# Performance work log

Measured on AMD Instinct MI355X. Metric: run time of the kernel, lower is better.

The kernel has to match this reference:

```python
import jax, jax.numpy as jnp
from jax import lax
import numpy as np

B, T = 16, 256
E, H, V = 512, 1024, 32000

def setup_inputs() -> dict:
    key = jax.random.key(0)
    ks = jax.random.split(key, 10)
    s = lambda fan_in: 1.0 / np.sqrt(fan_in)
    return {
        "z": jax.random.normal(ks[0], (B, H), dtype=jnp.float32),
        "x": jax.random.randint(ks[1], (B, T), 0, V, dtype=jnp.int64),
        "emb_table": jax.random.normal(ks[2], (V, E), dtype=jnp.float32) * 0.02,
        "W_init": jax.random.uniform(ks[3], (H, H), jnp.float32, -s(H), s(H)),
        "b_init": jnp.zeros((H,), jnp.float32),
        "W_ih": jax.random.uniform(ks[4], (3 * H, E), jnp.float32, -s(H), s(H)),
        "W_hh": jax.random.uniform(ks[5], (3 * H, H), jnp.float32, -s(H), s(H)),
        "b_ih": jax.random.uniform(ks[6], (3 * H,), jnp.float32, -s(H), s(H)),
        "b_hh": jax.random.uniform(ks[7], (3 * H,), jnp.float32, -s(H), s(H)),
        "W_out": jax.random.uniform(ks[8], (V, H), jnp.float32, -s(H), s(H)),
        "b_out": jnp.zeros((V,), jnp.float32),
    }

def reference(z, x, emb_table, W_init, b_init, W_ih, W_hh, b_ih, b_hh, W_out, b_out):
    # h0 = tanh(aff_init_lm(z))
    h0 = jnp.tanh(z @ W_init.T + b_init)  # [B, H]
    xe = emb_table[x]                      # [B, T, E] embedding lookup
    # Precompute input-side gate projections for all timesteps (no recurrence on input side)
    gi_all = jnp.einsum('bte,ge->btg', xe, W_ih) + b_ih  # [B, T, 3H]

    def step(h, gi):
        gh = h @ W_hh.T + b_hh                 # [B, 3H]
        ir, iz, inn = jnp.split(gi, 3, axis=-1)
        hr, hz, hn = jnp.split(gh, 3, axis=-1)
        r = jax.nn.sigmoid(ir + hr)
        zg = jax.nn.sigmoid(iz + hz)
        n = jnp.tanh(inn + r * hn)
        h_new = (1.0 - zg) * n + zg * h
        # Original module emits aff_out_x(h[j]) (state BEFORE consuming token j),
        # so we output the PREVIOUS hidden state at each step.
        return h_new, h

    _, hs_prev = lax.scan(step, h0, jnp.swapaxes(gi_all, 0, 1))  # [T, B, H] = h0..h_{T-1}
    hs = jnp.swapaxes(hs_prev, 0, 1)                              # [B, T, H]
    logits = jnp.einsum('bth,vh->btv', hs, W_out) + b_out         # [B, T, V]
    return logits
```

## Files before the change

### kernel.cpp

```cpp
#include <hip/hip_runtime.h>

typedef __attribute__((ext_vector_type(8))) short bf16x8;
typedef __attribute__((ext_vector_type(8))) unsigned short ushort8;
typedef __attribute__((ext_vector_type(4))) float f32x4;
typedef __attribute__((ext_vector_type(4))) int i32x4;

__device__ __forceinline__ unsigned short f2bf(float f) {
  union { float f; unsigned u; } v; v.f = f;
  unsigned r = (v.u + 0x7FFFu + ((v.u >> 16) & 1u)) >> 16;
  return (unsigned short)r;
}
__device__ __forceinline__ float bf2f(unsigned short h) {
  union { unsigned u; float f; } v; v.u = ((unsigned)h) << 16;
  return v.f;
}
__device__ __forceinline__ float sigm(float x) { return 1.f / (1.f + __expf(-x)); }
__device__ __forceinline__ float tanh_(float x) { return 1.f - 2.f / (__expf(2.f * x) + 1.f); }

__device__ __forceinline__ i32x4 ld_coh_b128(const void* p) {
  i32x4 r;
  asm volatile("global_load_dwordx4 %0, %1, off sc0 sc1" : "=v"(r) : "v"(p) : "memory");
  return r;
}
__device__ __forceinline__ void st_coh_b128(void* p, i32x4 v) {
  asm volatile("global_store_dwordx4 %0, %1, off sc0 sc1" :: "v"(p), "v"(v) : "memory");
}
__device__ __forceinline__ void st_coh_b16(void* p, unsigned v) {
  asm volatile("global_store_short %0, %1, off sc0 sc1" :: "v"(p), "v"(v) : "memory");
}
__device__ __forceinline__ void wait_vm0_fence() {
  asm volatile("s_waitcnt vmcnt(0)" ::: "memory");
  __builtin_amdgcn_sched_barrier(0);
}

#define GLDS(g, l) __builtin_amdgcn_global_load_lds( \
    (const __attribute__((address_space(1))) unsigned int*)(g), \
    (__attribute__((address_space(3))) unsigned int*)(l), 16, 0, 0)

__global__ __launch_bounds__(256) void prep(
    const int* __restrict__ x, const float* __restrict__ emb, unsigned short* __restrict__ xe,
    const float* __restrict__ z, const float* __restrict__ Wi, const float* __restrict__ bi,
    float* __restrict__ h0f, unsigned short* __restrict__ hb16,
    const float* __restrict__ Wih, unsigned short* __restrict__ WihB,
    const float* __restrict__ Wout, unsigned short* __restrict__ WoutB) {
  const int tid = threadIdx.x;
  const unsigned bid = blockIdx.x;
  if (bid < 2048) {
    const int m = (bid << 1) + (tid >> 7);
    const int tok = x[m];
    const int c = tid & 127;
    const float4 v = ((const float4*)(emb + (size_t)tok * 512))[c];
    ushort4 o; o.x = f2bf(v.x); o.y = f2bf(v.y); o.z = f2bf(v.z); o.w = f2bf(v.w);
    ((ushort4*)(xe + (size_t)m * 512))[c] = o;
  } else if (bid < 2112) {
    const int idx = (bid - 2048) * 256 + tid;
    const int b = idx & 15, i = idx >> 4;
    const float4* wr = (const float4*)(Wi + (size_t)i * 1024);
    const float4* zr = (const float4*)(z + (size_t)b * 1024);
    float acc = bi[i];
#pragma unroll 4
    for (int k = 0; k < 256; ++k) {
      float4 w = wr[k], zv = zr[k];
      acc += w.x * zv.x + w.y * zv.y + w.z * zv.z + w.w * zv.w;
    }
    const float h = tanh_(acc);
    h0f[(size_t)b * 1024 + i] = h;
    hb16[((i >> 4) << 8) + (b << 4) + (i & 15)] = f2bf(h);
  } else if (bid < 3648) {
    const int i = (int)(bid - 2112) * 256 + tid;
    const float4 v = ((const float4*)Wih)[i];
    ushort4 o; o.x = f2bf(v.x); o.y = f2bf(v.y); o.z = f2bf(v.z); o.w = f2bf(v.w);
    ((ushort4*)WihB)[i] = o;
  } else {
    for (int i = (int)(bid - 3648) * 256 + tid; i < 32000 * 1024 / 4; i += 512 * 256) {
      const float4 v = ((const float4*)Wout)[i];
      ushort4 o; o.x = f2bf(v.x); o.y = f2bf(v.y); o.z = f2bf(v.z); o.w = f2bf(v.w);
      ((ushort4*)WoutB)[i] = o;
    }
  }
}

__global__ __launch_bounds__(256) void gemm_bt(
    const unsigned short* __restrict__ A, const unsigned short* __restrict__ Bm,
    const float* __restrict__ bias, unsigned short* __restrict__ C,
    int M, int N, int K) {
  __shared__ __align__(16) unsigned short As[128 * 32];
  __shared__ __align__(16) unsigned short Bs[128 * 32];
  const int tid = threadIdx.x;
  const int lane = tid & 63, wave = tid >> 6;
  const int nTM = M >> 7;
  const int nwg = (int)gridDim.x;
  int wg = blockIdx.x;
  if ((nwg & 7) == 0) wg = (wg & 7) * (nwg >> 3) + (wg >> 3);
  const int bm = wg % nTM, bn = wg / nTM;
  const long row0 = (long)bm << 7, col0 = (long)bn << 7;
  const int wm = (wave & 1) << 6, wn = (wave >> 1) << 6;

  f32x4 acc[4][4] = {};

  const int sr = (wave << 4) + (lane >> 2);
  const int sk = (lane & 3) << 3;
  const unsigned short* Abase = A + ((size_t)(row0 + sr)) * K + sk;
  const unsigned short* Bbase = Bm + ((size_t)(col0 + sr)) * K + sk;
  char* ldsA = (char*)As + wave * 1024;
  char* ldsB = (char*)Bs + wave * 1024;

  for (int k0 = 0; k0 < K; k0 += 32) {
    __syncthreads();
    GLDS(Abase + k0, ldsA);
    GLDS(Abase + (size_t)64 * K + k0, ldsA + 4096);
    GLDS(Bbase + k0, ldsB);
    GLDS(Bbase + (size_t)64 * K + k0, ldsB + 4096);
    __syncthreads();
    const int lr = lane & 15, lk = (lane >> 4) << 3;
    bf16x8 af[4], bfr[4];
#pragma unroll
    for (int i = 0; i < 4; ++i) {
      af[i]  = *(const bf16x8*)(As + (wm + i * 16 + lr) * 32 + lk);
      bfr[i] = *(const bf16x8*)(Bs + (wn + i * 16 + lr) * 32 + lk);
    }
#pragma unroll
    for (int i = 0; i < 4; ++i)
#pragma unroll
      for (int j = 0; j < 4; ++j)
        acc[i][j] = __builtin_amdgcn_mfma_f32_16x16x32_bf16(af[i], bfr[j], acc[i][j], 0, 0, 0);
  }

  const int lr = lane & 15, lq = (lane >> 4) << 2;
#pragma unroll
  for (int i = 0; i < 4; ++i) {
#pragma unroll
    for (int q = 0; q < 4; ++q) {
      const long r = row0 + wm + i * 16 + lq + q;
      unsigned short* crow = C + (size_t)r * N;
#pragma unroll
      for (int j = 0; j < 4; ++j) {
        const long cc = col0 + wn + j * 16 + lr;
        crow[cc] = f2bf(acc[i][j][q] + bias[cc]);
      }
    }
  }
}

__global__ __launch_bounds__(512, 1) void mega(
    const float* __restrict__ Whh, const float* __restrict__ bhh,
    const unsigned short* __restrict__ gi, const float* __restrict__ h0f,
    unsigned short* __restrict__ hb16, unsigned short* __restrict__ hs,
    unsigned int* __restrict__ flags,
    const unsigned short* __restrict__ WoutB, const float* __restrict__ bout,
    float* __restrict__ out) {
  __shared__ __align__(16) char lds[65536];
  const int tid = threadIdx.x, lane = tid & 63, wave = tid >> 6;

  if (blockIdx.x < 64) {
    const int j = blockIdx.x;
    if (tid >= 256) {
      for (int t = 0; t < 256; ++t) { __syncthreads(); if (t < 255) __syncthreads(); }
      __syncthreads();
      return;
    }
    float (*ghp)[16][48] = (float (*)[16][48])lds;
    unsigned short (*hsl)[16] = (unsigned short (*)[16])(lds + 12288);

    const int lr = lane & 15;
    const int hi8 = (lane >> 4) << 3;
    const int kw = wave << 8;

    bf16x8 wf[3][8];
#pragma unroll
    for (int n = 0; n < 3; ++n) {
      const float* wrow = Whh + (size_t)(n * 1024 + (j << 4) + lr) * 1024 + kw + hi8;
#pragma unroll
      for (int ki = 0; ki < 8; ++ki) {
        const float4 u = *(const float4*)(wrow + ki * 32);
        const float4 v = *(const float4*)(wrow + ki * 32 + 4);
        bf16x8 w;
        w[0] = (short)f2bf(u.x); w[1] = (short)f2bf(u.y);
        w[2] = (short)f2bf(u.z); w[3] = (short)f2bf(u.w);
        w[4] = (short)f2bf(v.x); w[5] = (short)f2bf(v.y);
        w[6] = (short)f2bf(v.z); w[7] = (short)f2bf(v.w);
        wf[n][ki] = w;
      }
    }

    const int b = tid >> 4, c = tid & 15;
    const int cg = (j << 4) + c;
    float hreg = h0f[(size_t)b * 1024 + cg];
    const float br = bhh[cg], bz = bhh[1024 + cg], bn = bhh[2048 + cg];

    const unsigned short* gr0 = gi + ((size_t)b * 256 + 0) * 3072;
    float ir = bf2f(gr0[cg]), iz = bf2f(gr0[1024 + cg]), inn = bf2f(gr0[2048 + cg]);

    for (int t = 0; t < 256; ++t) {
      if (t > 0) {
        long guard = 0;
        for (;;) {
          const unsigned f = __hip_atomic_load(&flags[lane << 5], __ATOMIC_RELAXED,
                                               __HIP_MEMORY_SCOPE_AGENT);
          if (__all(f >= (unsigned)t)) break;
          __builtin_amdgcn_s_sleep(1);
          if (++guard > (1L << 20)) break;
        }
      }

      const unsigned short* base = hb16 + ((t & 1) << 14);
      i32x4 hv[8];
#pragma unroll
      for (int ki = 0; ki < 8; ++ki) {
        const int kk = kw + (ki << 5) + hi8;
        hv[ki] = ld_coh_b128(base + ((kk >> 4) << 8) + (lr << 4) + (kk & 15));
      }
      wait_vm0_fence();

      f32x4 acc[3] = {};
#pragma unroll
      for (int ki = 0; ki < 8; ++ki) {
        const bf16x8 af = __builtin_bit_cast(bf16x8, hv[ki]);
#pragma unroll
        for (int n = 0; n < 3; ++n)
          acc[n] = __builtin_amdgcn_mfma_f32_16x16x32_bf16(af, wf[n][ki], acc[n], 0, 0, 0);
      }
#pragma unroll
      for (int n = 0; n < 3; ++n)
#pragma unroll
        for (int q = 0; q < 4; ++q)
          ghp[wave][(lane >> 4) * 4 + q][n * 16 + lr] = acc[n][q];
      __syncthreads();

      const float hr = ghp[0][b][c]      + ghp[1][b][c]      + ghp[2][b][c]      + ghp[3][b][c];
      const float hz = ghp[0][b][16 + c] + ghp[1][b][16 + c] + ghp[2][b][16 + c] + ghp[3][b][16 + c];
      const float hn = ghp[0][b][32 + c] + ghp[1][b][32 + c] + ghp[2][b][32 + c] + ghp[3][b][32 + c];
      const float rg = sigm(ir + hr + br);
      const float zg = sigm(iz + hz + bz);
      const float ng = tanh_(inn + rg * (hn + bn));
      const float hprev = hreg;
      hreg = (1.f - zg) * ng + zg * hprev;

      if (t < 255) {
        hsl[b][c] = f2bf(hreg);
        __syncthreads();
        unsigned short* nb = hb16 + (((t + 1) & 1) << 14) + (j << 8);
        if (tid < 32) {
          const i32x4 v = *(const i32x4*)&hsl[tid >> 1][(tid & 1) << 3];
          st_coh_b128(nb + (tid << 3), v);
        }
        if (wave == 0)
          asm volatile("s_waitcnt vmcnt(0)" ::: "memory");
        if (tid == 0)
          __hip_atomic_store(&flags[j << 5], (unsigned)(t + 1),
                             __ATOMIC_RELAXED, __HIP_MEMORY_SCOPE_AGENT);
      }

      st_coh_b16(hs + ((size_t)((t << 4) + b) << 10) + cg, (unsigned)f2bf(hprev));
      if (t < 255) {
        const unsigned short* gr = gi + ((size_t)b * 256 + (t + 1)) * 3072;
        ir = bf2f(gr[cg]); iz = bf2f(gr[1024 + cg]); inn = bf2f(gr[2048 + cg]);
      }
    }
    asm volatile("s_waitcnt vmcnt(0)" ::: "memory");
    __syncthreads();
    if (tid == 0)
      __hip_atomic_store(&flags[j << 5], 1024u, __ATOMIC_RELAXED, __HIP_MEMORY_SCOPE_AGENT);
    return;
  }

  const int gb = blockIdx.x - 64;
  const int bm = gb / 125, bn = gb % 125;
  const long row0 = (long)bm << 8, col0 = (long)bn << 8;

  {
    unsigned thr = (unsigned)(16 * bm + 17); if (thr > 255u) thr = 1024u;
    if (wave == 0) {
      long guard = 0;
      for (;;) {
        const unsigned f = __hip_atomic_load(&flags[lane << 5], __ATOMIC_RELAXED,
                                             __HIP_MEMORY_SCOPE_AGENT);
        if (__all(f >= thr)) break;
        __builtin_amdgcn_s_sleep(32);
        if (++guard > (1L << 22)) break;
      }
    }
    __syncthreads();
  }

  const int wm = wave >> 2, wn = wave & 3;
  const int arow = tid >> 1, ahalf = (tid & 1) << 5;
  const char* Ab = (const char*)hs + ((row0 + arow) << 11) + ahalf;
  const int awz0 = ((arow << 6) + ahalf) ^ ((arow & 12) << 2);
  const int awz1 = ((arow << 6) + ahalf + 16) ^ ((arow & 12) << 2);
  const int srow = tid >> 2, skb = (tid & 3) << 4;
  auto stageB = [&](int sp, int rr) {
    const int row = (rr << 7) + srow;
    const int kbu = skb ^ ((row & 12) << 2);
    const char* g = (const char*)WoutB + ((col0 + row) << 11) + (sp << 6) + kbu;
    char* l = lds + ((sp & 1) << 15) + 16384 + (rr << 13) + (wave << 10);
    GLDS(g, l);
  };
  const int lr = lane & 15, ko = (lane >> 4) << 4;
  auto rdA = [&](int buf, int mrep) {
    const int rt = (wm << 7) + (mrep << 4) + lr;
    const int a = (rt << 6) + ko;
    return *(const bf16x8*)(lds + (buf << 15) + (a ^ ((rt & 12) << 2)));
  };
  auto rdB = [&](int buf, int nrep) {
    const int rt = (wn << 6) + (nrep << 4) + lr;
    const int a = (rt << 6) + ko;
    return *(const bf16x8*)(lds + (buf << 15) + 16384 + (a ^ ((rt & 12) << 2)));
  };

  f32x4 acc[8][4] = {};
  i32x4 rA0 = ld_coh_b128(Ab);
  i32x4 rA1 = ld_coh_b128(Ab + 16);
  stageB(0, 0); stageB(0, 1);

  for (int s = 0; s < 32; ++s) {
    const int buf = s & 1;
    if (s < 31) {
      stageB(s + 1, 0); stageB(s + 1, 1);
      asm volatile("s_waitcnt vmcnt(2)" ::: "memory");
    } else {
      asm volatile("s_waitcnt vmcnt(0)" ::: "memory");
    }
    __builtin_amdgcn_sched_barrier(0);
    *(i32x4*)(lds + (buf << 15) + awz0) = rA0;
    *(i32x4*)(lds + (buf << 15) + awz1) = rA1;
    if (s < 31) {
      rA0 = ld_coh_b128(Ab + ((s + 1) << 6));
      rA1 = ld_coh_b128(Ab + ((s + 1) << 6) + 16);
    }
    asm volatile("s_waitcnt lgkmcnt(0)" ::: "memory");
    __builtin_amdgcn_sched_barrier(0);
    __builtin_amdgcn_s_barrier();

    bf16x8 bfr[4], af[4], af2[4];
#pragma unroll
    for (int n = 0; n < 4; ++n) bfr[n] = rdB(buf, n);
#pragma unroll
    for (int m = 0; m < 4; ++m) af[m] = rdA(buf, m);
    asm volatile("s_waitcnt lgkmcnt(0)" ::: "memory");
    __builtin_amdgcn_sched_barrier(0);
    __builtin_amdgcn_s_setprio(1);
#pragma unroll
    for (int m = 0; m < 4; ++m)
#pragma unroll
      for (int n = 0; n < 4; ++n)
        acc[m][n] = __builtin_amdgcn_mfma_f32_16x16x32_bf16(af[m], bfr[n], acc[m][n], 0, 0, 0);
    __builtin_amdgcn_s_setprio(0);
#pragma unroll
    for (int m = 0; m < 4; ++m) af2[m] = rdA(buf, m + 4);
    asm volatile("s_waitcnt lgkmcnt(0)" ::: "memory");
    __builtin_amdgcn_sched_barrier(0);
    __builtin_amdgcn_s_barrier();
    __builtin_amdgcn_s_setprio(1);
#pragma unroll
    for (int m = 0; m < 4; ++m)
#pragma unroll
      for (int n = 0; n < 4; ++n)
        acc[m + 4][n] = __builtin_amdgcn_mfma_f32_16x16x32_bf16(af2[m], bfr[n], acc[m + 4][n], 0, 0, 0);
    __builtin_amdgcn_s_setprio(0);
  }

  const int lq = (lane >> 4) << 2;
#pragma unroll
  for (int mr = 0; mr < 8; ++mr) {
#pragma unroll
    for (int q = 0; q < 4; ++q) {
      const int ar = (int)row0 + (wm << 7) + (mr << 4) + lq + q;
      const int tt = ar >> 4, bb = ar & 15;
      float* crow = out + ((size_t)bb * 256 + tt) * 32000;
#pragma unroll
      for (int nr = 0; nr < 4; ++nr) {
        const long cc = col0 + (wn << 6) + (nr << 4) + lr;
        crow[cc] = acc[mr][nr][q] + bout[cc];
      }
    }
  }
}

extern "C" void kernel_launch(void* const* d_in, const int* in_sizes, int n_in,
                              void* d_out, int out_size, void* d_ws, size_t ws_size,
                              hipStream_t stream) {
  const float* z     = (const float*)d_in[0];
  const int*   x     = (const int*)d_in[1];
  const float* emb   = (const float*)d_in[2];
  const float* Winit = (const float*)d_in[3];
  const float* binit = (const float*)d_in[4];
  const float* Wih   = (const float*)d_in[5];
  const float* Whh   = (const float*)d_in[6];
  const float* bih   = (const float*)d_in[7];
  const float* bhh   = (const float*)d_in[8];
  const float* Wout  = (const float*)d_in[9];
  const float* bout  = (const float*)d_in[10];
  float* out = (float*)d_out;

  char* ws = (char*)d_ws;
  size_t off = 0;
  auto alloc = [&](size_t bytes) { void* p = ws + off; off += (bytes + 255) & ~(size_t)255; return p; };
  unsigned int*   flags = (unsigned int*)alloc(64 * 128);
  unsigned short* xe    = (unsigned short*)alloc((size_t)4096 * 512 * 2);
  unsigned short* WihB  = (unsigned short*)alloc((size_t)3072 * 512 * 2);
  unsigned short* WoutB = (unsigned short*)alloc((size_t)32000 * 1024 * 2);
  unsigned short* giB   = (unsigned short*)alloc((size_t)4096 * 3072 * 2);
  unsigned short* hsB   = (unsigned short*)alloc((size_t)4096 * 1024 * 2);
  float*          h0f   = (float*)alloc((size_t)16 * 1024 * 4);
  unsigned short* hb16  = (unsigned short*)alloc((size_t)2 * 16 * 1024 * 2);
  (void)ws_size; (void)in_sizes; (void)n_in; (void)out_size;

  hipMemsetAsync(flags, 0, 64 * 128, stream);

  prep<<<dim3(4160), 256, 0, stream>>>(x, emb, xe, z, Winit, binit, h0f, hb16,
                                       Wih, WihB, Wout, WoutB);

  gemm_bt<<<dim3(32 * 24), 256, 0, stream>>>(xe, WihB, bih, giB, 4096, 3072, 512);

  mega<<<dim3(2064), 512, 0, stream>>>(Whh, bhh, giB, h0f, hb16, hsB, flags,
                                       WoutB, bout, out);
}
```

Measured before the change: 867.6 us.

## Replace flag-based step sync with tagged hidden-state words in triple buffer

Each hidden-state element is stored as a 32-bit word holding the bf16 value in the high half and the timestep tag in the low half, in a triple-buffered exchange area. Consumer blocks poll the data directly until every tag matches the current step, so the separate flag round trip and the LDS staging with a cross-block barrier before publishing go away. The cost is that each step moves twice as many bytes, readers spin on the data itself, and a fallback to the old flag wait remains for stalls.

```diff
diff --git a/kernel.cpp b/kernel.cpp
--- a/kernel.cpp
+++ b/kernel.cpp
@@ -22,8 +22,8 @@
   asm volatile("global_load_dwordx4 %0, %1, off sc0 sc1" : "=v"(r) : "v"(p) : "memory");
   return r;
 }
-__device__ __forceinline__ void st_coh_b128(void* p, i32x4 v) {
-  asm volatile("global_store_dwordx4 %0, %1, off sc0 sc1" :: "v"(p), "v"(v) : "memory");
+__device__ __forceinline__ void st_coh_b32(void* p, unsigned v) {
+  asm volatile("global_store_dword %0, %1, off sc0 sc1" :: "v"(p), "v"(v) : "memory");
 }
 __device__ __forceinline__ void st_coh_b16(void* p, unsigned v) {
   asm volatile("global_store_short %0, %1, off sc0 sc1" :: "v"(p), "v"(v) : "memory");
@@ -40,7 +40,7 @@
 __global__ __launch_bounds__(256) void prep(
     const int* __restrict__ x, const float* __restrict__ emb, unsigned short* __restrict__ xe,
     const float* __restrict__ z, const float* __restrict__ Wi, const float* __restrict__ bi,
-    float* __restrict__ h0f, unsigned short* __restrict__ hb16,
+    float* __restrict__ h0f, unsigned* __restrict__ hbt,
     const float* __restrict__ Wih, unsigned short* __restrict__ WihB,
     const float* __restrict__ Wout, unsigned short* __restrict__ WoutB) {
   const int tid = threadIdx.x;
@@ -65,7 +65,7 @@
     }
     const float h = tanh_(acc);
     h0f[(size_t)b * 1024 + i] = h;
-    hb16[((i >> 4) << 8) + (b << 4) + (i & 15)] = f2bf(h);
+    hbt[((i >> 4) << 8) + (b << 4) + (i & 15)] = ((unsigned)f2bf(h) << 16);
   } else if (bid < 3648) {
     const int i = (int)(bid - 2112) * 256 + tid;
     const float4 v = ((const float4*)Wih)[i];
@@ -145,7 +145,7 @@
 __global__ __launch_bounds__(512, 1) void mega(
     const float* __restrict__ Whh, const float* __restrict__ bhh,
     const unsigned short* __restrict__ gi, const float* __restrict__ h0f,
-    unsigned short* __restrict__ hb16, unsigned short* __restrict__ hs,
+    unsigned* __restrict__ hbt, unsigned short* __restrict__ hs,
     unsigned int* __restrict__ flags,
     const unsigned short* __restrict__ WoutB, const float* __restrict__ bout,
     float* __restrict__ out) {
@@ -160,7 +160,6 @@
       return;
     }
     float (*ghp)[16][48] = (float (*)[16][48])lds;
-    unsigned short (*hsl)[16] = (unsigned short (*)[16])(lds + 12288);
 
     const int lr = lane & 15;
     const int hi8 = (lane >> 4) << 3;
@@ -191,8 +190,31 @@
     const unsigned short* gr0 = gi + ((size_t)b * 256 + 0) * 3072;
     float ir = bf2f(gr0[cg]), iz = bf2f(gr0[1024 + cg]), inn = bf2f(gr0[2048 + cg]);
 
+    int slot = 0;
+    i32x4 v[16];
     for (int t = 0; t < 256; ++t) {
-      if (t > 0) {
+      const unsigned* hsrc = hbt + slot * 16384;
+      auto tagread = [&]() -> bool {
+#pragma unroll
+        for (int ki = 0; ki < 8; ++ki) {
+          const int kk = kw + (ki << 5) + hi8;
+          const unsigned* p0 = hsrc + ((kk >> 4) << 8) + (lr << 4) + (kk & 15);
+          v[2 * ki]     = ld_coh_b128(p0);
+          v[2 * ki + 1] = ld_coh_b128(p0 + 4);
+        }
+        wait_vm0_fence();
+        unsigned bad = 0;
+#pragma unroll
+        for (int o = 0; o < 16; ++o)
+#pragma unroll
+          for (int d = 0; d < 4; ++d)
+            bad |= ((unsigned)v[o][d] ^ (unsigned)t) & 0xFFFFu;
+        return __all(bad == 0);
+      };
+
+      bool ok = false;
+      for (int tries = 0; tries < 1024 && !ok; ++tries) ok = tagread();
+      if (!ok) {
         long guard = 0;
         for (;;) {
           const unsigned f = __hip_atomic_load(&flags[lane << 5], __ATOMIC_RELAXED,
@@ -201,21 +223,21 @@
           __builtin_amdgcn_s_sleep(1);
           if (++guard > (1L << 20)) break;
         }
-      }
-
-      const unsigned short* base = hb16 + ((t & 1) << 14);
-      i32x4 hv[8];
+        for (long g2 = 0; g2 < (1L << 20); ++g2) {
+          if (tagread()) break;
+          __builtin_amdgcn_s_sleep(1);
+        }
+      }
+
+      f32x4 acc[3] = {};
 #pragma unroll
       for (int ki = 0; ki < 8; ++ki) {
-        const int kk = kw + (ki << 5) + hi8;
-        hv[ki] = ld_coh_b128(base + ((kk >> 4) << 8) + (lr << 4) + (kk & 15));
-      }
-      wait_vm0_fence();
-
-      f32x4 acc[3] = {};
-#pragma unroll
-      for (int ki = 0; ki < 8; ++ki) {
-        const bf16x8 af = __builtin_bit_cast(bf16x8, hv[ki]);
+        i32x4 p;
+        p[0] = (int)(((unsigned)v[2 * ki][0] >> 16)     | ((unsigned)v[2 * ki][1] & 0xFFFF0000u));
+        p[1] = (int)(((unsigned)v[2 * ki][2] >> 16)     | ((unsigned)v[2 * ki][3] & 0xFFFF0000u));
+        p[2] = (int)(((unsigned)v[2 * ki + 1][0] >> 16) | ((unsigned)v[2 * ki + 1][1] & 0xFFFF0000u));
+        p[3] = (int)(((unsigned)v[2 * ki + 1][2] >> 16) | ((unsigned)v[2 * ki + 1][3] & 0xFFFF0000u));
+        const bf16x8 af = __builtin_bit_cast(bf16x8, p);
 #pragma unroll
         for (int n = 0; n < 3; ++n)
           acc[n] = __builtin_amdgcn_mfma_f32_16x16x32_bf16(af, wf[n][ki], acc[n], 0, 0, 0);
@@ -236,26 +258,23 @@
       const float hprev = hreg;
       hreg = (1.f - zg) * ng + zg * hprev;
 
+      const int slot_w = (slot == 2) ? 0 : slot + 1;
       if (t < 255) {
-        hsl[b][c] = f2bf(hreg);
+        st_coh_b32(hbt + slot_w * 16384 + (j << 8) + (b << 4) + c,
+                   ((unsigned)f2bf(hreg) << 16) | (unsigned)(t + 1));
+      }
+      st_coh_b16(hs + ((size_t)((t << 4) + b) << 10) + cg, (unsigned)f2bf(hprev));
+
+      if (t < 255) {
+        asm volatile("s_waitcnt vmcnt(0)" ::: "memory");
         __syncthreads();
-        unsigned short* nb = hb16 + (((t + 1) & 1) << 14) + (j << 8);
-        if (tid < 32) {
-          const i32x4 v = *(const i32x4*)&hsl[tid >> 1][(tid & 1) << 3];
-          st_coh_b128(nb + (tid << 3), v);
-        }
-        if (wave == 0)
-          asm volatile("s_waitcnt vmcnt(0)" ::: "memory");
         if (tid == 0)
           __hip_atomic_store(&flags[j << 5], (unsigned)(t + 1),
                              __ATOMIC_RELAXED, __HIP_MEMORY_SCOPE_AGENT);
-      }
-
-      st_coh_b16(hs + ((size_t)((t << 4) + b) << 10) + cg, (unsigned)f2bf(hprev));
-      if (t < 255) {
         const unsigned short* gr = gi + ((size_t)b * 256 + (t + 1)) * 3072;
         ir = bf2f(gr[cg]); iz = bf2f(gr[1024 + cg]); inn = bf2f(gr[2048 + cg]);
       }
+      slot = slot_w;
     }
     asm volatile("s_waitcnt vmcnt(0)" ::: "memory");
     __syncthreads();
@@ -397,22 +416,23 @@
   size_t off = 0;
   auto alloc = [&](size_t bytes) { void* p = ws + off; off += (bytes + 255) & ~(size_t)255; return p; };
   unsigned int*   flags = (unsigned int*)alloc(64 * 128);
+  unsigned*       hbt   = (unsigned*)alloc((size_t)3 * 16384 * 4);
   unsigned short* xe    = (unsigned short*)alloc((size_t)4096 * 512 * 2);
   unsigned short* WihB  = (unsigned short*)alloc((size_t)3072 * 512 * 2);
   unsigned short* WoutB = (unsigned short*)alloc((size_t)32000 * 1024 * 2);
   unsigned short* giB   = (unsigned short*)alloc((size_t)4096 * 3072 * 2);
   unsigned short* hsB   = (unsigned short*)alloc((size_t)4096 * 1024 * 2);
   float*          h0f   = (float*)alloc((size_t)16 * 1024 * 4);
-  unsigned short* hb16  = (unsigned short*)alloc((size_t)2 * 16 * 1024 * 2);
   (void)ws_size; (void)in_sizes; (void)n_in; (void)out_size;
 
   hipMemsetAsync(flags, 0, 64 * 128, stream);
-
-  prep<<<dim3(4160), 256, 0, stream>>>(x, emb, xe, z, Winit, binit, h0f, hb16,
+  hipMemsetAsync((char*)hbt + 65536, 0xAA, 131072, stream);
+
+  prep<<<dim3(4160), 256, 0, stream>>>(x, emb, xe, z, Winit, binit, h0f, hbt,
                                        Wih, WihB, Wout, WoutB);
 
   gemm_bt<<<dim3(32 * 24), 256, 0, stream>>>(xe, WihB, bih, giB, 4096, 3072, 512);
 
-  mega<<<dim3(2064), 512, 0, stream>>>(Whh, bhh, giB, h0f, hb16, hsB, flags,
+  mega<<<dim3(2064), 512, 0, stream>>>(Whh, bhh, giB, h0f, hbt, hsB, flags,
                                        WoutB, bout, out);
 }
```

Measured after the change: 937.9 us. 8.1% more time.

## Fuse input-projection GEMM into persistent mega kernel with per-tile readiness counters

Applied to the files above, without the earlier changes.

Removes the separate gemm_bt launch and runs the input-gate projection tiles as extra workgroups inside the mega kernel. The embedding rows are reordered to time-major so each 128-row tile covers 8 timesteps, and each tile bumps a per-tile counter that the recurrence blocks poll before consuming gi for step t. The aim is to overlap the input GEMM with the start of the GRU recurrence and drop a launch boundary. In exchange the recurrence spin-loop gains an extra atomic poll, and the gi loads are now issued inside the step instead of being prefetched one step ahead.

```diff
diff --git a/kernel.cpp b/kernel.cpp
--- a/kernel.cpp
+++ b/kernel.cpp
@@ -20,6 +20,11 @@
 __device__ __forceinline__ i32x4 ld_coh_b128(const void* p) {
   i32x4 r;
   asm volatile("global_load_dwordx4 %0, %1, off sc0 sc1" : "=v"(r) : "v"(p) : "memory");
+  return r;
+}
+__device__ __forceinline__ unsigned ld_coh_u16(const void* p) {
+  unsigned r;
+  asm volatile("global_load_ushort %0, %1, off sc0 sc1" : "=v"(r) : "v"(p) : "memory");
   return r;
 }
 __device__ __forceinline__ void st_coh_b128(void* p, i32x4 v) {
@@ -46,12 +51,13 @@
   const int tid = threadIdx.x;
   const unsigned bid = blockIdx.x;
   if (bid < 2048) {
-    const int m = (bid << 1) + (tid >> 7);
-    const int tok = x[m];
+    const int r = (bid << 1) + (tid >> 7);
+    const int b = r & 15, t = r >> 4;
+    const int tok = x[b * 256 + t];
     const int c = tid & 127;
     const float4 v = ((const float4*)(emb + (size_t)tok * 512))[c];
     ushort4 o; o.x = f2bf(v.x); o.y = f2bf(v.y); o.z = f2bf(v.z); o.w = f2bf(v.w);
-    ((ushort4*)(xe + (size_t)m * 512))[c] = o;
+    ((ushort4*)(xe + (size_t)r * 512))[c] = o;
   } else if (bid < 2112) {
     const int idx = (bid - 2048) * 256 + tid;
     const int b = idx & 15, i = idx >> 4;
@@ -80,73 +86,13 @@
   }
 }
 
-__global__ __launch_bounds__(256) void gemm_bt(
-    const unsigned short* __restrict__ A, const unsigned short* __restrict__ Bm,
-    const float* __restrict__ bias, unsigned short* __restrict__ C,
-    int M, int N, int K) {
-  __shared__ __align__(16) unsigned short As[128 * 32];
-  __shared__ __align__(16) unsigned short Bs[128 * 32];
-  const int tid = threadIdx.x;
-  const int lane = tid & 63, wave = tid >> 6;
-  const int nTM = M >> 7;
-  const int nwg = (int)gridDim.x;
-  int wg = blockIdx.x;
-  if ((nwg & 7) == 0) wg = (wg & 7) * (nwg >> 3) + (wg >> 3);
-  const int bm = wg % nTM, bn = wg / nTM;
-  const long row0 = (long)bm << 7, col0 = (long)bn << 7;
-  const int wm = (wave & 1) << 6, wn = (wave >> 1) << 6;
-
-  f32x4 acc[4][4] = {};
-
-  const int sr = (wave << 4) + (lane >> 2);
-  const int sk = (lane & 3) << 3;
-  const unsigned short* Abase = A + ((size_t)(row0 + sr)) * K + sk;
-  const unsigned short* Bbase = Bm + ((size_t)(col0 + sr)) * K + sk;
-  char* ldsA = (char*)As + wave * 1024;
-  char* ldsB = (char*)Bs + wave * 1024;
-
-  for (int k0 = 0; k0 < K; k0 += 32) {
-    __syncthreads();
-    GLDS(Abase + k0, ldsA);
-    GLDS(Abase + (size_t)64 * K + k0, ldsA + 4096);
-    GLDS(Bbase + k0, ldsB);
-    GLDS(Bbase + (size_t)64 * K + k0, ldsB + 4096);
-    __syncthreads();
-    const int lr = lane & 15, lk = (lane >> 4) << 3;
-    bf16x8 af[4], bfr[4];
-#pragma unroll
-    for (int i = 0; i < 4; ++i) {
-      af[i]  = *(const bf16x8*)(As + (wm + i * 16 + lr) * 32 + lk);
-      bfr[i] = *(const bf16x8*)(Bs + (wn + i * 16 + lr) * 32 + lk);
-    }
-#pragma unroll
-    for (int i = 0; i < 4; ++i)
-#pragma unroll
-      for (int j = 0; j < 4; ++j)
-        acc[i][j] = __builtin_amdgcn_mfma_f32_16x16x32_bf16(af[i], bfr[j], acc[i][j], 0, 0, 0);
-  }
-
-  const int lr = lane & 15, lq = (lane >> 4) << 2;
-#pragma unroll
-  for (int i = 0; i < 4; ++i) {
-#pragma unroll
-    for (int q = 0; q < 4; ++q) {
-      const long r = row0 + wm + i * 16 + lq + q;
-      unsigned short* crow = C + (size_t)r * N;
-#pragma unroll
-      for (int j = 0; j < 4; ++j) {
-        const long cc = col0 + wn + j * 16 + lr;
-        crow[cc] = f2bf(acc[i][j][q] + bias[cc]);
-      }
-    }
-  }
-}
-
 __global__ __launch_bounds__(512, 1) void mega(
     const float* __restrict__ Whh, const float* __restrict__ bhh,
-    const unsigned short* __restrict__ gi, const float* __restrict__ h0f,
+    unsigned short* __restrict__ gi, const float* __restrict__ h0f,
     unsigned short* __restrict__ hb16, unsigned short* __restrict__ hs,
-    unsigned int* __restrict__ flags,
+    unsigned int* __restrict__ flags, unsigned int* __restrict__ gicnt,
+    const unsigned short* __restrict__ xe, const unsigned short* __restrict__ WihB,
+    const float* __restrict__ bih,
     const unsigned short* __restrict__ WoutB, const float* __restrict__ bout,
     float* __restrict__ out) {
   __shared__ __align__(16) char lds[65536];
@@ -188,16 +134,20 @@
     float hreg = h0f[(size_t)b * 1024 + cg];
     const float br = bhh[cg], bz = bhh[1024 + cg], bn = bhh[2048 + cg];
 
-    const unsigned short* gr0 = gi + ((size_t)b * 256 + 0) * 3072;
-    float ir = bf2f(gr0[cg]), iz = bf2f(gr0[1024 + cg]), inn = bf2f(gr0[2048 + cg]);
-
     for (int t = 0; t < 256; ++t) {
-      if (t > 0) {
+      {
         long guard = 0;
         for (;;) {
-          const unsigned f = __hip_atomic_load(&flags[lane << 5], __ATOMIC_RELAXED,
-                                               __HIP_MEMORY_SCOPE_AGENT);
-          if (__all(f >= (unsigned)t)) break;
+          bool ok = true;
+          if (t > 0) {
+            const unsigned f = __hip_atomic_load(&flags[lane << 5], __ATOMIC_RELAXED,
+                                                 __HIP_MEMORY_SCOPE_AGENT);
+            ok = (f >= (unsigned)t);
+          }
+          const unsigned g2 = __hip_atomic_load(&gicnt[(t >> 3) << 5], __ATOMIC_RELAXED,
+                                                __HIP_MEMORY_SCOPE_AGENT);
+          ok = ok && (g2 >= 24u);
+          if (__all(ok)) break;
           __builtin_amdgcn_s_sleep(1);
           if (++guard > (1L << 20)) break;
         }
@@ -210,6 +160,10 @@
         const int kk = kw + (ki << 5) + hi8;
         hv[ki] = ld_coh_b128(base + ((kk >> 4) << 8) + (lr << 4) + (kk & 15));
       }
+      const char* gbase = (const char*)gi + ((size_t)((t << 4) + b) * 3072 + cg) * 2;
+      const unsigned uir = ld_coh_u16(gbase);
+      const unsigned uiz = ld_coh_u16(gbase + 2048);
+      const unsigned uin = ld_coh_u16(gbase + 4096);
       wait_vm0_fence();
 
       f32x4 acc[3] = {};
@@ -227,6 +181,9 @@
           ghp[wave][(lane >> 4) * 4 + q][n * 16 + lr] = acc[n][q];
       __syncthreads();
 
+      const float ir = bf2f((unsigned short)uir);
+      const float iz = bf2f((unsigned short)uiz);
+      const float inn = bf2f((unsigned short)uin);
       const float hr = ghp[0][b][c]      + ghp[1][b][c]      + ghp[2][b][c]      + ghp[3][b][c];
       const float hz = ghp[0][b][16 + c] + ghp[1][b][16 + c] + ghp[2][b][16 + c] + ghp[3][b][16 + c];
       const float hn = ghp[0][b][32 + c] + ghp[1][b][32 + c] + ghp[2][b][32 + c] + ghp[3][b][32 + c];
@@ -252,10 +209,6 @@
       }
 
       st_coh_b16(hs + ((size_t)((t << 4) + b) << 10) + cg, (unsigned)f2bf(hprev));
-      if (t < 255) {
-        const unsigned short* gr = gi + ((size_t)b * 256 + (t + 1)) * 3072;
-        ir = bf2f(gr[cg]); iz = bf2f(gr[1024 + cg]); inn = bf2f(gr[2048 + cg]);
-      }
     }
     asm volatile("s_waitcnt vmcnt(0)" ::: "memory");
     __syncthreads();
@@ -264,7 +217,72 @@
     return;
   }
 
-  const int gb = blockIdx.x - 64;
+  if (blockIdx.x < 832) {
+    const int g = blockIdx.x - 64;
+    const int tm = g / 24, tn = g % 24;
+    const long row0 = (long)tm << 7, col0 = (long)tn << 7;
+    char* As = lds;
+    char* Bs = lds + 8192;
+    char* Ct = lds + 16384;
+
+    const int sr = tid >> 2, sk = (tid & 3) << 3;
+    const unsigned short* Abase = xe + (row0 + sr) * 512 + sk;
+    const unsigned short* Bbase = WihB + (col0 + sr) * 512 + sk;
+    char* ldsA = As + wave * 1024;
+    char* ldsB = Bs + wave * 1024;
+
+    const int wm2 = (wave >> 2) << 6, wn2 = (wave & 3) << 5;
+    const int lr = lane & 15, lk = (lane >> 4) << 3;
+    f32x4 acc[4][2] = {};
+
+    for (int k0 = 0; k0 < 512; k0 += 32) {
+      __syncthreads();
+      GLDS(Abase + k0, ldsA);
+      GLDS(Bbase + k0, ldsB);
+      __syncthreads();
+      bf16x8 af[4], bfr[2];
+#pragma unroll
+      for (int i = 0; i < 4; ++i)
+        af[i] = *(const bf16x8*)(As + ((wm2 + i * 16 + lr) * 32 + lk) * 2);
+#pragma unroll
+      for (int jj = 0; jj < 2; ++jj)
+        bfr[jj] = *(const bf16x8*)(Bs + ((wn2 + jj * 16 + lr) * 32 + lk) * 2);
+#pragma unroll
+      for (int i = 0; i < 4; ++i)
+#pragma unroll
+        for (int jj = 0; jj < 2; ++jj)
+          acc[i][jj] = __builtin_amdgcn_mfma_f32_16x16x32_bf16(af[i], bfr[jj], acc[i][jj], 0, 0, 0);
+    }
+
+    const int lq = (lane >> 4) << 2;
+    float bias0 = bih[col0 + wn2 + lr], bias1 = bih[col0 + wn2 + 16 + lr];
+    __syncthreads();
+#pragma unroll
+    for (int i = 0; i < 4; ++i)
+#pragma unroll
+      for (int jj = 0; jj < 2; ++jj)
+#pragma unroll
+        for (int q = 0; q < 4; ++q)
+          *(unsigned short*)(Ct + (wm2 + i * 16 + lq + q) * 256
+                                + ((wn2 + jj * 16 + lr) << 1)) =
+              f2bf(acc[i][jj][q] + (jj ? bias1 : bias0));
+    __syncthreads();
+#pragma unroll
+    for (int k2 = 0; k2 < 4; ++k2) {
+      const int s2 = (k2 << 9) + tid;
+      const int row = s2 >> 4, colb = (s2 & 15) << 4;
+      st_coh_b128((char*)gi + (size_t)(row0 + row) * 6144 + (col0 << 1) + colb,
+                  *(const i32x4*)(Ct + row * 256 + colb));
+    }
+    asm volatile("s_waitcnt vmcnt(0)" ::: "memory");
+    __syncthreads();
+    if (tid == 0)
+      __hip_atomic_fetch_add(&gicnt[tm << 5], 1u, __ATOMIC_RELAXED,
+                             __HIP_MEMORY_SCOPE_AGENT);
+    return;
+  }
+
+  const int gb = blockIdx.x - 832;
   const int bm = gb / 125, bn = gb % 125;
   const long row0 = (long)bm << 8, col0 = (long)bn << 8;
 
@@ -397,6 +415,7 @@
   size_t off = 0;
   auto alloc = [&](size_t bytes) { void* p = ws + off; off += (bytes + 255) & ~(size_t)255; return p; };
   unsigned int*   flags = (unsigned int*)alloc(64 * 128);
+  unsigned int*   gicnt = (unsigned int*)alloc(32 * 128);
   unsigned short* xe    = (unsigned short*)alloc((size_t)4096 * 512 * 2);
   unsigned short* WihB  = (unsigned short*)alloc((size_t)3072 * 512 * 2);
   unsigned short* WoutB = (unsigned short*)alloc((size_t)32000 * 1024 * 2);
@@ -406,13 +425,11 @@
   unsigned short* hb16  = (unsigned short*)alloc((size_t)2 * 16 * 1024 * 2);
   (void)ws_size; (void)in_sizes; (void)n_in; (void)out_size;
 
-  hipMemsetAsync(flags, 0, 64 * 128, stream);
+  hipMemsetAsync(flags, 0, 64 * 128 + 32 * 128, stream);
 
   prep<<<dim3(4160), 256, 0, stream>>>(x, emb, xe, z, Winit, binit, h0f, hb16,
                                        Wih, WihB, Wout, WoutB);
 
-  gemm_bt<<<dim3(32 * 24), 256, 0, stream>>>(xe, WihB, bih, giB, 4096, 3072, 512);
-
-  mega<<<dim3(2064), 512, 0, stream>>>(Whh, bhh, giB, h0f, hb16, hsB, flags,
-                                       WoutB, bout, out);
-}
+  mega<<<dim3(2832), 512, 0, stream>>>(Whh, bhh, giB, h0f, hb16, hsB, flags, gicnt,
+                                       xe, WihB, bih, WoutB, bout, out);
+}
```

Result: slower. 1.012 ms (+16.7%).
